# Kernel optimization log

Hardware: AMD Instinct MI355X
Metric: run time of the kernel (lower is better)

## Reference

```python
import jax, jax.numpy as jnp
import numpy as np

S, N, L, B = 200000, 250000, 64, 64


def setup_inputs() -> dict:
    key = jax.random.key(0)
    k = jax.random.split(key, 7)
    return {
        "We_m": jax.random.normal(k[0], (S, L), jnp.float32) * 0.02,
        "be_m": jax.random.normal(k[1], (L,), jnp.float32) * 0.02,
        "Wd_m": jax.random.normal(k[2], (L, S), jnp.float32) * 0.02,
        "bd_m": jax.random.normal(k[3], (S,), jnp.float32) * 0.02,
        "x": jax.random.normal(k[4], (B, N), jnp.float32),
        "nn_n": jax.random.randint(k[5], (N,), 0, S),  # nearest master node for each new node
        "nn_m": jax.random.randint(k[6], (S,), 0, N),  # nearest new node for each master node
    }


def _reshape_weights(We_m, be_m, Wd_m, bd_m, nn_n, nn_m):
    # Vectorized equivalent of GFN_AE.reshape_weights(expand=True, agglomerate=True,
    # update_master=False, eval mode).
    s, l = We_m.shape
    n = nn_n.shape[0]
    # Expand: new node pt_n is "added" iff nn_m[nn_n[pt_n]] != pt_n.
    added = (nn_m[nn_n] != jnp.arange(n)).astype(We_m.dtype)  # [N]
    # Sequential We_i[pt_m] *= c/(c+1) collapses to division by (c_m + 1),
    # c_m = number of added new nodes whose nearest master node is m.
    c_m = jax.ops.segment_sum(added, nn_n, num_segments=s)  # [S]
    We_s = We_m / (c_m + 1.0)[:, None]  # scaled master encoder rows
    # Appended row i (for added node pt_n, src m = nn_n[pt_n]) equals We_s[m],
    # Wd column / bd entry copied from m; its nn_m_ext entry is pt_n itself.
    # Agglomerate: We_n sums contributors, Wd_n/bd_n take the running mean (= plain mean).
    We_n = jax.ops.segment_sum(We_s, nn_m, num_segments=n) + added[:, None] * We_s[nn_n]
    WdT = Wd_m.T  # [S, L]
    cnt = jax.ops.segment_sum(jnp.ones((s,), We_m.dtype), nn_m, num_segments=n) + added
    denom = jnp.maximum(cnt, 1.0)
    Wd_n = ((jax.ops.segment_sum(WdT, nn_m, num_segments=n) + added[:, None] * WdT[nn_n]) / denom[:, None]).T  # [L, N]
    bd_n = (jax.ops.segment_sum(bd_m, nn_m, num_segments=n) + added * bd_m[nn_n]) / denom  # [N]
    return We_n, Wd_n, bd_n


def reference(We_m, be_m, Wd_m, bd_m, x, nn_n, nn_m):
    We_n, Wd_n, bd_n = _reshape_weights(We_m, be_m, Wd_m, bd_m, nn_n, nn_m)
    z = x @ We_n + be_m            # encode: [B, N] x [N, L]
    out = z @ Wd_n + bd_n          # decode: [B, L] x [L, N]
    return out
```

## Files before the change

kernel.cpp:

```cpp
#include <hip/hip_runtime.h>

constexpr int S_ = 200000;
constexpr int N_ = 250000;

constexpr int NCHUNK = (N_ + 63) / 64;
constexpr int ENC_BLOCKS = (NCHUNK + 3) / 4;
constexpr int WEN_BLOCKS = NCHUNK * 2;
constexpr int DEC_BLOCKS = (N_ + 31) / 32;

constexpr int EMASK = 0x3FFFF;

typedef __attribute__((ext_vector_type(8))) short bf16x8;
typedef __attribute__((ext_vector_type(4))) float f32x4;
typedef __attribute__((ext_vector_type(4))) unsigned short us4;
typedef __attribute__((ext_vector_type(8))) unsigned short us8;

__global__ void k_added_counts(const int* __restrict__ nn_n, const int* __restrict__ nn_m,
                               int* __restrict__ added, int* __restrict__ c_m,
                               int* __restrict__ ecnt) {
    int i = blockIdx.x * 256 + threadIdx.x;
    if (i < N_) {
        int m = nn_n[i];
        int a = (nn_m[m] != i) ? 1 : 0;
        added[i] = a;
        if (a) {
            atomicAdd(&c_m[m], 1);
            atomicAdd(&ecnt[i], 1);
        }
    }
    if (i < S_) {
        atomicAdd(&ecnt[nn_m[i]], 1);
    }
}

__global__ void k_scan_blocksum(const int* __restrict__ ecnt, int* __restrict__ bsum) {
    __shared__ int sd[256];
    int b = blockIdx.x, t = threadIdx.x;
    int base = b * 1024 + t * 4;
    int s = 0;
#pragma unroll
    for (int k = 0; k < 4; k++) { int idx = base + k; if (idx < N_) s += ecnt[idx]; }
    sd[t] = s;
    __syncthreads();
    for (int off = 128; off > 0; off >>= 1) {
        if (t < off) sd[t] += sd[t + off];
        __syncthreads();
    }
    if (t == 0) bsum[b] = sd[0];
}

__global__ void k_scan_apply(const int* __restrict__ ecnt, const int* __restrict__ bsum,
                             int* __restrict__ offs) {
    __shared__ int sd[256];
    __shared__ int sp[256];
    int b = blockIdx.x, t = threadIdx.x;
    sp[t] = (t < b) ? bsum[t] : 0;
    __syncthreads();
    for (int off = 128; off > 0; off >>= 1) {
        if (t < off) sp[t] += sp[t + off];
        __syncthreads();
    }
    int prev = sp[0];

    int base = b * 1024 + t * 4;
    int v[4]; int s = 0;
#pragma unroll
    for (int k = 0; k < 4; k++) { int idx = base + k; v[k] = (idx < N_) ? ecnt[idx] : 0; s += v[k]; }
    sd[t] = s;
    __syncthreads();
    for (int off = 1; off < 256; off <<= 1) {
        int xv = (t >= off) ? sd[t - off] : 0;
        __syncthreads();
        sd[t] += xv;
        __syncthreads();
    }
    int run = prev + sd[t] - s;
#pragma unroll
    for (int k = 0; k < 4; k++) {
        int idx = base + k;
        if (idx < N_) offs[idx] = run;
        run += v[k];
    }
}

__global__ void k_fill(const int* __restrict__ nn_m, const int* __restrict__ nn_n,
                       const int* __restrict__ added, const int* __restrict__ offs,
                       const int* __restrict__ c_m,
                       int* __restrict__ fill, int* __restrict__ elist) {
    int i = blockIdx.x * 256 + threadIdx.x;
    if (i < S_) {
        int j = nn_m[i];
        int p = atomicAdd(&fill[j], 1);
        elist[offs[j] + p] = i | (c_m[i] << 18);
    }
    if (i < N_ && added[i]) {
        int m = nn_n[i];
        int p = atomicAdd(&fill[i], 1);
        elist[offs[i] + p] = m | (c_m[m] << 18);
    }
}

__global__ __launch_bounds__(256) void k_wen(
        const float* __restrict__ We_m,
        const int* __restrict__ ecnt, const int* __restrict__ offs,
        const int* __restrict__ elist, unsigned short* __restrict__ Wf) {
    __shared__ unsigned short sw[4096];
    int t = threadIdx.x;
    int lane = t & 63;
    int wv = __builtin_amdgcn_readfirstlane(t >> 6);
    int b = blockIdx.x;
    int jb = b * 32 + wv * 8;
    int c[8], o[8], cl[8];
    float acc[8];
#pragma unroll
    for (int s = 0; s < 8; s++) {
        int j = jb + s;
        bool v = (j < N_);
        c[s] = v ? __builtin_amdgcn_readfirstlane(ecnt[j]) : 0;
        o[s] = v ? __builtin_amdgcn_readfirstlane(offs[j]) : 0;
        cl[s] = max(c[s] - 1, 0);
        acc[s] = 0.f;
    }
    int cmax = 0;
#pragma unroll
    for (int s = 0; s < 8; s++) cmax = max(cmax, c[s]);

    if (cmax > 0) {
        int e[8];
#pragma unroll
        for (int s = 0; s < 8; s++)
            e[s] = __builtin_amdgcn_readfirstlane(elist[o[s]]);
        for (int q = 0; q < cmax; q++) {
            int en[8];
#pragma unroll
            for (int s = 0; s < 8; s++) {
                int p = o[s] + min(q + 1, cl[s]);
                en[s] = __builtin_amdgcn_readfirstlane(elist[p]);
            }
            int mm[8]; float sc[8];
#pragma unroll
            for (int s = 0; s < 8; s++) {
                bool valid = (q < c[s]);
                mm[s] = valid ? (e[s] & EMASK) : 0;
                float r = __builtin_amdgcn_rcpf((float)((e[s] >> 18) + 1));
                sc[s] = valid ? r : 0.0f;
            }
            float row[8];
#pragma unroll
            for (int s = 0; s < 8; s++)
                row[s] = We_m[(size_t)mm[s] * 64 + lane];
#pragma unroll
            for (int s = 0; s < 8; s++)
                acc[s] += row[s] * sc[s];
#pragma unroll
            for (int s = 0; s < 8; s++) e[s] = en[s];
        }
    }

    int ct = lane >> 4, l15 = lane & 15;
    us8 hv, lv;
#pragma unroll
    for (int s = 0; s < 8; s++) {
        float v = acc[s];
        unsigned u = __float_as_uint(v);
        hv[s] = (unsigned short)(u >> 16);
        float r = v - __uint_as_float(u & 0xffff0000u);
        lv[s] = (unsigned short)(__float_as_uint(r) >> 16);
    }
    int base = ct * 1024 + (l15 + 16 * wv) * 8;
    *(us8*)&sw[base]       = hv;
    *(us8*)&sw[base + 512] = lv;
    __syncthreads();
    int ch = b >> 1, sH = b & 1;
    size_t R = ((size_t)ch * 2 + sH) * 4096;
#pragma unroll
    for (int r = 0; r < 2; r++) {
        int idx = r * 2048 + t * 8;
        *(us8*)(Wf + R + idx) = *(const us8*)&sw[idx];
    }
}

__global__ __launch_bounds__(256) void k_encode(const float* __restrict__ x,
        const unsigned short* __restrict__ Wf, float* __restrict__ zp2) {
    int t = threadIdx.x;
    int lane = t & 63;
    int wv = t >> 6;
    int mrow = lane & 15;
    int kq = lane >> 4;
    const float* xbase = x + (size_t)(wv * 16 + mrow) * N_ + kq * 8;
    f32x4 acc[4];
#pragma unroll
    for (int ct = 0; ct < 4; ct++) acc[ct] = (f32x4){0.f, 0.f, 0.f, 0.f};

    for (int cc = 0; cc < 4; cc++) {
        int c = blockIdx.x * 4 + cc;
        if (c >= NCHUNK) break;
        int n0 = c * 64;
#pragma unroll
        for (int s = 0; s < 2; s++) {
            float av[8];
            if (n0 + s * 32 + kq * 8 + 8 <= N_) {
                float4 a0 = *(const float4*)(xbase + n0 + s * 32);
                float4 a1 = *(const float4*)(xbase + n0 + s * 32 + 4);
                av[0] = a0.x; av[1] = a0.y; av[2] = a0.z; av[3] = a0.w;
                av[4] = a1.x; av[5] = a1.y; av[6] = a1.z; av[7] = a1.w;
            } else {
#pragma unroll
                for (int i = 0; i < 8; i++) av[i] = 0.f;
            }
            const bf16x8* bp = (const bf16x8*)Wf + ((size_t)c * 2 + s) * 512 + lane;
            bf16x8 bh[4], bl[4];
#pragma unroll
            for (int ct = 0; ct < 4; ct++) {
                bh[ct] = bp[ct * 128];
                bl[ct] = bp[ct * 128 + 64];
            }
            bf16x8 ah, al;
#pragma unroll
            for (int i = 0; i < 8; i++) {
                float v = av[i];
                unsigned u = __float_as_uint(v);
                ah[i] = (short)(u >> 16);
                float r = v - __uint_as_float(u & 0xffff0000u);
                al[i] = (short)(__float_as_uint(r) >> 16);
            }
#pragma unroll
            for (int ct = 0; ct < 4; ct++) {
                acc[ct] = __builtin_amdgcn_mfma_f32_16x16x32_bf16(ah, bh[ct], acc[ct], 0, 0, 0);
                acc[ct] = __builtin_amdgcn_mfma_f32_16x16x32_bf16(al, bh[ct], acc[ct], 0, 0, 0);
                acc[ct] = __builtin_amdgcn_mfma_f32_16x16x32_bf16(ah, bl[ct], acc[ct], 0, 0, 0);
            }
        }
    }

    int row = blockIdx.x & 63;
    float* zr = zp2 + row * 4096;
#pragma unroll
    for (int ct = 0; ct < 4; ct++) {
#pragma unroll
        for (int r = 0; r < 4; r++) {
            int b = wv * 16 + kq * 4 + r;
            int l = ct * 16 + mrow;
            atomicAdd(&zr[b * 64 + l], acc[ct][r]);
        }
    }
}

__global__ void k_zred(const float* __restrict__ zp2, const float* __restrict__ be_m,
                       float* __restrict__ z2g) {
    int slot = blockIdx.x * 256 + threadIdx.x;
    float s = 0.f;
    for (int r = 0; r < 64; r++) s += zp2[r * 4096 + slot];
    int b = slot >> 6, l = slot & 63;
    z2g[l * 64 + b] = s + be_m[l];
}

__global__ __launch_bounds__(256) void k_pmat(
        const float* __restrict__ Wd_m, const float* __restrict__ bd_m,
        const float* __restrict__ z2g, float* __restrict__ P) {
    __shared__ float ws[64 * 64];
    int t = threadIdx.x;
    int m0 = blockIdx.x * 64;
#pragma unroll
    for (int r = 0; r < 4; r++) {
        int flat = r * 256 + t;
        int l = flat >> 4;
        int c4 = flat & 15;
        float4 v = *(const float4*)&Wd_m[(size_t)l * S_ + m0 + c4 * 4];
        *(float4*)&ws[l * 64 + c4 * 4] = v;
    }
    __syncthreads();

    int m = t & 63;
    int bg = __builtin_amdgcn_readfirstlane(t >> 6);
    float bd = bd_m[m0 + m];
    float acc[16];
#pragma unroll
    for (int q = 0; q < 16; q++) acc[q] = bd;
    const float* zb = z2g + bg * 16;
#pragma unroll 4
    for (int l = 0; l < 64; l++) {
        float w = ws[l * 64 + m];
        const float* zr = zb + l * 64;
#pragma unroll
        for (int q = 0; q < 16; q++) acc[q] += w * zr[q];
    }

    float4* Pv = (float4*)&P[(size_t)(m0 + m) * 64 + bg * 16];
#pragma unroll
    for (int q4 = 0; q4 < 4; q4++)
        Pv[q4] = make_float4(acc[q4 * 4 + 0], acc[q4 * 4 + 1],
                             acc[q4 * 4 + 2], acc[q4 * 4 + 3]);
}

__global__ __launch_bounds__(256) void k_decode(const float* __restrict__ P,
        const int* __restrict__ ecnt, const int* __restrict__ offs,
        const int* __restrict__ elist, float* __restrict__ out) {
    __shared__ float tile[32][65];
    int t = threadIdx.x;
    int wv = __builtin_amdgcn_readfirstlane(t >> 6);
    int lane = t & 63;
    int j0 = blockIdx.x * 32;
    int jb = j0 + wv * 8;
    int c[8], o[8], cl[8];
    float acc[8];
#pragma unroll
    for (int s = 0; s < 8; s++) {
        int j = jb + s;
        bool v = (j < N_);
        c[s] = v ? __builtin_amdgcn_readfirstlane(ecnt[j]) : 0;
        o[s] = v ? __builtin_amdgcn_readfirstlane(offs[j]) : 0;
        cl[s] = max(c[s] - 1, 0);
        acc[s] = 0.f;
    }
    int cmax = 0;
#pragma unroll
    for (int s = 0; s < 8; s++) cmax = max(cmax, c[s]);

    if (cmax > 0) {
        int e[8];
#pragma unroll
        for (int s = 0; s < 8; s++)
            e[s] = __builtin_amdgcn_readfirstlane(elist[o[s]]);
        for (int q = 0; q < cmax; q++) {
            int en[8];
#pragma unroll
            for (int s = 0; s < 8; s++) {
                int p = o[s] + min(q + 1, cl[s]);
                en[s] = __builtin_amdgcn_readfirstlane(elist[p]);
            }
            int mm[8]; float sc[8];
#pragma unroll
            for (int s = 0; s < 8; s++) {
                bool valid = (q < c[s]);
                mm[s] = valid ? (e[s] & EMASK) : 0;
                sc[s] = valid ? 1.0f : 0.0f;
            }
            float row[8];
#pragma unroll
            for (int s = 0; s < 8; s++)
                row[s] = P[(size_t)mm[s] * 64 + lane];
#pragma unroll
            for (int s = 0; s < 8; s++)
                acc[s] += row[s] * sc[s];
#pragma unroll
            for (int s = 0; s < 8; s++) e[s] = en[s];
        }
    }
#pragma unroll
    for (int s = 0; s < 8; s++) {
        int cc = (c[s] > 1) ? c[s] : 1;
        tile[wv * 8 + s][lane] = acc[s] * (1.0f / (float)cc);
    }
    __syncthreads();
#pragma unroll
    for (int r = 0; r < 8; r++) {
        int b = r * 8 + (t >> 5);
        int j = j0 + (t & 31);
        if (j < N_) out[(size_t)b * N_ + j] = tile[t & 31][b];
    }
}

extern "C" void kernel_launch(void* const* d_in, const int* in_sizes, int n_in,
                              void* d_out, int out_size, void* d_ws, size_t ws_size,
                              hipStream_t stream) {
    const float* We_m = (const float*)d_in[0];
    const float* be_m = (const float*)d_in[1];
    const float* Wd_m = (const float*)d_in[2];
    const float* bd_m = (const float*)d_in[3];
    const float* x    = (const float*)d_in[4];
    const int*   nn_n = (const int*)d_in[5];
    const int*   nn_m = (const int*)d_in[6];
    float* out = (float*)d_out;
    char* ws = (char*)d_ws;

    unsigned short* Wf = (unsigned short*)(ws + 0);
    float* P     = (float*)(ws + 0);
    int*   c_m   = (int*)(ws + 64012288);
    int*   ecnt  = (int*)(ws + 64812288);
    int*   fill  = (int*)(ws + 65812288);
    int*   added = (int*)(ws + 66812288);
    int*   offs  = (int*)(ws + 67812288);
    int*   elist = (int*)(ws + 68812288);
    float* zp2   = (float*)(ws + 70812288);
    float* z2g   = (float*)(ws + 71860864);
    int*   bsum  = (int*)(ws + 71877248);

    hipMemsetAsync(ws + 64012288, 0, 2800000, stream);
    hipMemsetAsync(zp2, 0, 1048576, stream);

    k_added_counts<<<977, 256, 0, stream>>>(nn_n, nn_m, added, c_m, ecnt);
    k_scan_blocksum<<<245, 256, 0, stream>>>(ecnt, bsum);
    k_scan_apply<<<245, 256, 0, stream>>>(ecnt, bsum, offs);
    k_fill<<<977, 256, 0, stream>>>(nn_m, nn_n, added, offs, c_m, fill, elist);
    k_wen<<<WEN_BLOCKS, 256, 0, stream>>>(We_m, ecnt, offs, elist, Wf);
    k_encode<<<ENC_BLOCKS, 256, 0, stream>>>(x, Wf, zp2);
    k_zred<<<16, 256, 0, stream>>>(zp2, be_m, z2g);
    k_pmat<<<3125, 256, 0, stream>>>(Wd_m, bd_m, z2g, P);
    k_decode<<<DEC_BLOCKS, 256, 0, stream>>>(P, ecnt, offs, elist, out);
}
```

Baseline: 350.7 us.

## Fuse We_n gather into encode kernel via shared-memory bf16 split tiles

Merges the We_n gather/agglomeration kernel with the encode MFMA kernel. Each block now gathers the We_m rows for its two 64-node chunks, splits them into hi/lo bf16 in LDS, and feeds the MFMAs straight from LDS. This drops the global Wf write and reload and one launch. The cost is that the gather latency now sits inside the encode loop, behind extra barriers, and each block covers 2 chunks instead of 4, which doubles the atomic partial-sum traffic into zp2.

```diff
diff --git a/kernel.cpp b/kernel.cpp
--- a/kernel.cpp
+++ b/kernel.cpp
@@ -4,15 +4,13 @@
 constexpr int N_ = 250000;
 
 constexpr int NCHUNK = (N_ + 63) / 64;
-constexpr int ENC_BLOCKS = (NCHUNK + 3) / 4;
-constexpr int WEN_BLOCKS = NCHUNK * 2;
+constexpr int FUSE_BLOCKS = (NCHUNK + 1) / 2;
 constexpr int DEC_BLOCKS = (N_ + 31) / 32;
 
 constexpr int EMASK = 0x3FFFF;
 
 typedef __attribute__((ext_vector_type(8))) short bf16x8;
 typedef __attribute__((ext_vector_type(4))) float f32x4;
-typedef __attribute__((ext_vector_type(4))) unsigned short us4;
 typedef __attribute__((ext_vector_type(8))) unsigned short us8;
 
 __global__ void k_added_counts(const int* __restrict__ nn_n, const int* __restrict__ nn_m,
@@ -100,102 +98,92 @@
     }
 }
 
-__global__ __launch_bounds__(256) void k_wen(
-        const float* __restrict__ We_m,
+__global__ __launch_bounds__(256) void k_wenc(
+        const float* __restrict__ x, const float* __restrict__ We_m,
         const int* __restrict__ ecnt, const int* __restrict__ offs,
-        const int* __restrict__ elist, unsigned short* __restrict__ Wf) {
-    __shared__ unsigned short sw[4096];
+        const int* __restrict__ elist, float* __restrict__ zp2) {
+    __shared__ unsigned short sw[8192];
     int t = threadIdx.x;
     int lane = t & 63;
     int wv = __builtin_amdgcn_readfirstlane(t >> 6);
-    int b = blockIdx.x;
-    int jb = b * 32 + wv * 8;
-    int c[8], o[8], cl[8];
-    float acc[8];
-#pragma unroll
-    for (int s = 0; s < 8; s++) {
-        int j = jb + s;
-        bool v = (j < N_);
-        c[s] = v ? __builtin_amdgcn_readfirstlane(ecnt[j]) : 0;
-        o[s] = v ? __builtin_amdgcn_readfirstlane(offs[j]) : 0;
-        cl[s] = max(c[s] - 1, 0);
-        acc[s] = 0.f;
-    }
-    int cmax = 0;
-#pragma unroll
-    for (int s = 0; s < 8; s++) cmax = max(cmax, c[s]);
-
-    if (cmax > 0) {
-        int e[8];
-#pragma unroll
-        for (int s = 0; s < 8; s++)
-            e[s] = __builtin_amdgcn_readfirstlane(elist[o[s]]);
-        for (int q = 0; q < cmax; q++) {
-            int en[8];
-#pragma unroll
-            for (int s = 0; s < 8; s++) {
-                int p = o[s] + min(q + 1, cl[s]);
-                en[s] = __builtin_amdgcn_readfirstlane(elist[p]);
-            }
-            int mm[8]; float sc[8];
-#pragma unroll
-            for (int s = 0; s < 8; s++) {
-                bool valid = (q < c[s]);
-                mm[s] = valid ? (e[s] & EMASK) : 0;
-                float r = __builtin_amdgcn_rcpf((float)((e[s] >> 18) + 1));
-                sc[s] = valid ? r : 0.0f;
-            }
-            float row[8];
-#pragma unroll
-            for (int s = 0; s < 8; s++)
-                row[s] = We_m[(size_t)mm[s] * 64 + lane];
-#pragma unroll
-            for (int s = 0; s < 8; s++)
-                acc[s] += row[s] * sc[s];
-#pragma unroll
-            for (int s = 0; s < 8; s++) e[s] = en[s];
-        }
-    }
-
-    int ct = lane >> 4, l15 = lane & 15;
-    us8 hv, lv;
-#pragma unroll
-    for (int s = 0; s < 8; s++) {
-        float v = acc[s];
-        unsigned u = __float_as_uint(v);
-        hv[s] = (unsigned short)(u >> 16);
-        float r = v - __uint_as_float(u & 0xffff0000u);
-        lv[s] = (unsigned short)(__float_as_uint(r) >> 16);
-    }
-    int base = ct * 1024 + (l15 + 16 * wv) * 8;
-    *(us8*)&sw[base]       = hv;
-    *(us8*)&sw[base + 512] = lv;
-    __syncthreads();
-    int ch = b >> 1, sH = b & 1;
-    size_t R = ((size_t)ch * 2 + sH) * 4096;
-#pragma unroll
-    for (int r = 0; r < 2; r++) {
-        int idx = r * 2048 + t * 8;
-        *(us8*)(Wf + R + idx) = *(const us8*)&sw[idx];
-    }
-}
-
-__global__ __launch_bounds__(256) void k_encode(const float* __restrict__ x,
-        const unsigned short* __restrict__ Wf, float* __restrict__ zp2) {
-    int t = threadIdx.x;
-    int lane = t & 63;
-    int wv = t >> 6;
     int mrow = lane & 15;
     int kq = lane >> 4;
+    int ct = lane >> 4, l15 = lane & 15;
     const float* xbase = x + (size_t)(wv * 16 + mrow) * N_ + kq * 8;
     f32x4 acc[4];
 #pragma unroll
-    for (int ct = 0; ct < 4; ct++) acc[ct] = (f32x4){0.f, 0.f, 0.f, 0.f};
-
-    for (int cc = 0; cc < 4; cc++) {
-        int c = blockIdx.x * 4 + cc;
-        if (c >= NCHUNK) break;
-        int n0 = c * 64;
+    for (int i = 0; i < 4; i++) acc[i] = (f32x4){0.f, 0.f, 0.f, 0.f};
+
+    for (int cc = 0; cc < 2; cc++) {
+        int chk = blockIdx.x * 2 + cc;
+        if (chk >= NCHUNK) break;
+        int n0 = chk * 64;
+
+        __syncthreads();
+        for (int g = 0; g < 2; g++) {
+            int jb = n0 + wv * 16 + g * 8;
+            int c[8], o[8], cl[8];
+            float ag[8];
+#pragma unroll
+            for (int s = 0; s < 8; s++) {
+                int j = jb + s;
+                bool v = (j < N_);
+                c[s] = v ? __builtin_amdgcn_readfirstlane(ecnt[j]) : 0;
+                o[s] = v ? __builtin_amdgcn_readfirstlane(offs[j]) : 0;
+                cl[s] = max(c[s] - 1, 0);
+                ag[s] = 0.f;
+            }
+            int cmax = 0;
+#pragma unroll
+            for (int s = 0; s < 8; s++) cmax = max(cmax, c[s]);
+            if (cmax > 0) {
+                int e[8];
+#pragma unroll
+                for (int s = 0; s < 8; s++)
+                    e[s] = __builtin_amdgcn_readfirstlane(elist[o[s]]);
+                for (int q = 0; q < cmax; q++) {
+                    int en[8];
+#pragma unroll
+                    for (int s = 0; s < 8; s++) {
+                        int p = o[s] + min(q + 1, cl[s]);
+                        en[s] = __builtin_amdgcn_readfirstlane(elist[p]);
+                    }
+                    int mm[8]; float sc[8];
+#pragma unroll
+                    for (int s = 0; s < 8; s++) {
+                        bool valid = (q < c[s]);
+                        mm[s] = valid ? (e[s] & EMASK) : 0;
+                        float r = __builtin_amdgcn_rcpf((float)((e[s] >> 18) + 1));
+                        sc[s] = valid ? r : 0.0f;
+                    }
+                    float row[8];
+#pragma unroll
+                    for (int s = 0; s < 8; s++)
+                        row[s] = We_m[(size_t)mm[s] * 64 + lane];
+#pragma unroll
+                    for (int s = 0; s < 8; s++)
+                        ag[s] += row[s] * sc[s];
+#pragma unroll
+                    for (int s = 0; s < 8; s++) e[s] = en[s];
+                }
+            }
+            us8 hv, lv;
+#pragma unroll
+            for (int s = 0; s < 8; s++) {
+                float v = ag[s];
+                unsigned u = __float_as_uint(v);
+                hv[s] = (unsigned short)(u >> 16);
+                float r = v - __uint_as_float(u & 0xffff0000u);
+                lv[s] = (unsigned short)(__float_as_uint(r) >> 16);
+            }
+            int kq2 = (wv & 1) * 2 + g;
+            int sH = wv >> 1;
+            int base = sH * 4096 + ct * 1024 + (l15 + 16 * kq2) * 8;
+            *(us8*)&sw[base]       = hv;
+            *(us8*)&sw[base + 512] = lv;
+        }
+        __syncthreads();
+
 #pragma unroll
         for (int s = 0; s < 2; s++) {
             float av[8];
@@ -208,12 +196,11 @@
 #pragma unroll
                 for (int i = 0; i < 8; i++) av[i] = 0.f;
             }
-            const bf16x8* bp = (const bf16x8*)Wf + ((size_t)c * 2 + s) * 512 + lane;
             bf16x8 bh[4], bl[4];
 #pragma unroll
-            for (int ct = 0; ct < 4; ct++) {
-                bh[ct] = bp[ct * 128];
-                bl[ct] = bp[ct * 128 + 64];
+            for (int c2 = 0; c2 < 4; c2++) {
+                bh[c2] = *(const bf16x8*)&sw[s * 4096 + c2 * 1024 + lane * 8];
+                bl[c2] = *(const bf16x8*)&sw[s * 4096 + c2 * 1024 + 512 + lane * 8];
             }
             bf16x8 ah, al;
 #pragma unroll
@@ -225,10 +212,10 @@
                 al[i] = (short)(__float_as_uint(r) >> 16);
             }
 #pragma unroll
-            for (int ct = 0; ct < 4; ct++) {
-                acc[ct] = __builtin_amdgcn_mfma_f32_16x16x32_bf16(ah, bh[ct], acc[ct], 0, 0, 0);
-                acc[ct] = __builtin_amdgcn_mfma_f32_16x16x32_bf16(al, bh[ct], acc[ct], 0, 0, 0);
-                acc[ct] = __builtin_amdgcn_mfma_f32_16x16x32_bf16(ah, bl[ct], acc[ct], 0, 0, 0);
+            for (int c2 = 0; c2 < 4; c2++) {
+                acc[c2] = __builtin_amdgcn_mfma_f32_16x16x32_bf16(ah, bh[c2], acc[c2], 0, 0, 0);
+                acc[c2] = __builtin_amdgcn_mfma_f32_16x16x32_bf16(al, bh[c2], acc[c2], 0, 0, 0);
+                acc[c2] = __builtin_amdgcn_mfma_f32_16x16x32_bf16(ah, bl[c2], acc[c2], 0, 0, 0);
             }
         }
     }
@@ -236,12 +223,12 @@
     int row = blockIdx.x & 63;
     float* zr = zp2 + row * 4096;
 #pragma unroll
-    for (int ct = 0; ct < 4; ct++) {
+    for (int c2 = 0; c2 < 4; c2++) {
 #pragma unroll
         for (int r = 0; r < 4; r++) {
             int b = wv * 16 + kq * 4 + r;
-            int l = ct * 16 + mrow;
-            atomicAdd(&zr[b * 64 + l], acc[ct][r]);
+            int l = c2 * 16 + mrow;
+            atomicAdd(&zr[b * 64 + l], acc[c2][r]);
         }
     }
 }
@@ -374,7 +361,6 @@
     float* out = (float*)d_out;
     char* ws = (char*)d_ws;
 
-    unsigned short* Wf = (unsigned short*)(ws + 0);
     float* P     = (float*)(ws + 0);
     int*   c_m   = (int*)(ws + 64012288);
     int*   ecnt  = (int*)(ws + 64812288);
@@ -393,8 +379,7 @@
     k_scan_blocksum<<<245, 256, 0, stream>>>(ecnt, bsum);
     k_scan_apply<<<245, 256, 0, stream>>>(ecnt, bsum, offs);
     k_fill<<<977, 256, 0, stream>>>(nn_m, nn_n, added, offs, c_m, fill, elist);
-    k_wen<<<WEN_BLOCKS, 256, 0, stream>>>(We_m, ecnt, offs, elist, Wf);
-    k_encode<<<ENC_BLOCKS, 256, 0, stream>>>(x, Wf, zp2);
+    k_wenc<<<FUSE_BLOCKS, 256, 0, stream>>>(x, We_m, ecnt, offs, elist, zp2);
     k_zred<<<16, 256, 0, stream>>>(zp2, be_m, z2g);
     k_pmat<<<3125, 256, 0, stream>>>(Wd_m, bd_m, z2g, P);
     k_decode<<<DEC_BLOCKS, 256, 0, stream>>>(P, ecnt, offs, elist, out);
```

Measured after the change: 331.1 us. 1.06x faster.
